# Kernel tuning notes

Measured on AMD Instinct MI355X. Metric: run time of the kernel, lower is better.

Reference implementation:

```python
import jax, jax.numpy as jnp
import numpy as np

N_HEAD = 16
D_HEAD = 64  # d_model=1024 // n_head=16


def setup_inputs() -> dict:
    key = jax.random.key(0)
    ks = jax.random.split(key, 8)
    B, S, D = 2, 2048, 1024
    scale = 1.0 / np.sqrt(D)
    return {
        "q": jax.random.normal(ks[0], (B, S, D), jnp.float32),
        "k": jax.random.normal(ks[1], (B, S, D), jnp.float32),
        "v": jax.random.normal(ks[2], (B, S, D), jnp.float32),
        "w_q": jax.random.normal(ks[3], (D, D), jnp.float32) * scale,
        "w_k": jax.random.normal(ks[4], (D, D), jnp.float32) * scale,
        "w_v": jax.random.normal(ks[5], (D, D), jnp.float32) * scale,
        "w_fc": jax.random.normal(ks[6], (D, D), jnp.float32) * scale,
        "b_fc": jnp.zeros((D,), jnp.float32),
    }


def reference(q, k, v, w_q, w_k, w_v, w_fc, b_fc):
    B, Sq, D = q.shape
    # projections (torch Linear: x @ W.T), split into heads -> [B, H, S, Dh]
    def proj(x, w):
        return (x @ w.T).reshape(B, x.shape[1], N_HEAD, D_HEAD).transpose(0, 2, 1, 3)
    qh, kh, vh = proj(q, w_q), proj(k, w_k), proj(v, w_v)
    # scaled dot-product attention with explicit weights (dropout = identity, eval mode)
    scores = jnp.einsum("bhqd,bhkd->bhqk", qh, kh) / jnp.sqrt(jnp.float32(D_HEAD))
    attn = jax.nn.softmax(scores, axis=-1)  # [B, H, Sq, Sk]
    ctx = jnp.einsum("bhqk,bhkd->bhqd", attn, vh)
    ctx = ctx.transpose(0, 2, 1, 3).reshape(B, Sq, D)
    out = ctx @ w_fc.T + b_fc
    return out, attn
```

## Files before the change

### kernel.cpp

```cpp
#include <hip/hip_runtime.h>


using f16   = _Float16;
using f16x4 = __attribute__((ext_vector_type(4))) f16;
using f16x8 = __attribute__((ext_vector_type(8))) f16;
using f32x4 = __attribute__((ext_vector_type(4))) float;

#define MFMA16(a, b, c) __builtin_amdgcn_mfma_f32_16x16x32_f16((a), (b), (c), 0, 0, 0)

__device__ static inline float fexp2(float x) {
#if __has_builtin(__builtin_amdgcn_exp2f)
  return __builtin_amdgcn_exp2f(x);
#else
  return exp2f(x);
#endif
}

#define C1 0.18033688011112042f

#define WAIT_BARRIER(IMM)                                              \
  do {                                                                 \
    asm volatile("s_waitcnt vmcnt(" #IMM ") lgkmcnt(0)" ::: "memory"); \
    __builtin_amdgcn_s_barrier();                                      \
  } while (0)

__device__ static inline void gld16(const void* gptr, void* lptr) {
  __builtin_amdgcn_global_load_lds(
      (const __attribute__((address_space(1))) void*)gptr,
      (__attribute__((address_space(3))) void*)lptr, 16, 0, 0);
}

__device__ static inline unsigned int pack2(float a, float b) {
  union { f16 h[2]; unsigned int u; } x;
  x.h[0] = (f16)a; x.h[1] = (f16)b;
  return x.u;
}

__global__ __launch_bounds__(256) void cast_all(
    const float* __restrict__ q, const float* __restrict__ k,
    const float* __restrict__ v, const float* __restrict__ wq,
    const float* __restrict__ wk, const float* __restrict__ wv,
    const float* __restrict__ wfc, f16* __restrict__ ws) {
  int i = blockIdx.x * 256 + threadIdx.x;
  const float* src;
  f16* dst;
  int li;
  if (i < 3145728) {
    if (i < 1048576)      { src = q; dst = ws;            li = i; }
    else if (i < 2097152) { src = k; dst = ws + 4194304;  li = i - 1048576; }
    else                  { src = v; dst = ws + 8388608;  li = i - 2097152; }
  } else {
    int j = i - 3145728;
    int wsel = j >> 18;
    src = (wsel == 0) ? wq : (wsel == 1) ? wk : (wsel == 2) ? wv : wfc;
    dst = ws + 12582912 + wsel * 1048576;
    li = j & 262143;
  }
  float4 x = ((const float4*)src)[li];
  f16x4 y;
  y[0] = (f16)x.x; y[1] = (f16)x.y; y[2] = (f16)x.z; y[3] = (f16)x.w;
  ((f16x4*)dst)[li] = y;
}

template <int MODE, int BN>
__global__ __launch_bounds__(256) void gemm_bt(
    const f16* __restrict__ A0, const f16* __restrict__ W0,
    const float* __restrict__ bias, void* __restrict__ Cout) {
  constexpr int FJ = BN / 32;
  __shared__ unsigned short XA[8192];
  __shared__ unsigned short WB[BN * 64];
  int tid = threadIdx.x;
  int w = tid >> 6, l = tid & 63, lq = l & 15, g = l >> 4;
  int nb3 = blockIdx.x * BN, mb = blockIdx.y * 128;
  int wsel = (MODE == 4) ? (nb3 >> 10) : 0;
  int nb = (MODE == 4) ? (nb3 & 1023) : nb3;
  const f16* A = (MODE == 4) ? A0 + (size_t)wsel * 4194304 : A0;
  const f16* W = (MODE == 4) ? W0 + (size_t)wsel * 1048576 : W0;
  bool swapR = (MODE == 4) && (wsel == 2);
  int wi = w >> 1, wj = w & 1;

  f32x4 acc[4][FJ];
#pragma unroll
  for (int i = 0; i < 4; i++)
#pragma unroll
    for (int j = 0; j < FJ; j++) acc[i][j] = (f32x4){0.f, 0.f, 0.f, 0.f};

  char* Xb = (char*)XA;
  char* Wb = (char*)WB;
  int row = tid >> 3;
  int c = (tid & 7) ^ (row & 7);
  const f16* Asrc = A + (size_t)(mb + row) * 1024 + c * 8;
  const f16* Wsrc = W + (size_t)(nb + row) * 1024 + c * 8;

  for (int k0 = 0; k0 < 1024; k0 += 64) {
#pragma unroll
    for (int i2 = 0; i2 < 4; i2++)
      gld16(Asrc + k0 + i2 * 32 * 1024, Xb + i2 * 4096 + w * 1024);
#pragma unroll
    for (int i2 = 0; i2 < BN / 32; i2++)
      gld16(Wsrc + k0 + i2 * 32 * 1024, Wb + i2 * 4096 + w * 1024);
    __syncthreads();

    const char* at = swapR ? Wb : Xb;
    const char* bt = swapR ? Xb : Wb;

    f16x8 bfr[FJ][2];
#pragma unroll
    for (int f = 0; f < FJ; f++) {
      int r = wj * (BN / 2) + f * 16 + lq;
      int sw = (r & 7) << 4;
      bfr[f][0] = *(const f16x8*)(bt + r * 128 + ((g * 16) ^ sw));
      bfr[f][1] = *(const f16x8*)(bt + r * 128 + ((64 + g * 16) ^ sw));
    }
#pragma unroll
    for (int fi = 0; fi < 4; fi++) {
      int r = wi * 64 + fi * 16 + lq;
      int sw = (r & 7) << 4;
      f16x8 a0 = *(const f16x8*)(at + r * 128 + ((g * 16) ^ sw));
      f16x8 a1 = *(const f16x8*)(at + r * 128 + ((64 + g * 16) ^ sw));
#pragma unroll
      for (int fj = 0; fj < FJ; fj++) {
        acc[fi][fj] = MFMA16(a0, bfr[fj][0], acc[fi][fj]);
        acc[fi][fj] = MFMA16(a1, bfr[fj][1], acc[fi][fj]);
      }
    }
    __syncthreads();
  }

#pragma unroll
  for (int fi = 0; fi < 4; fi++) {
#pragma unroll
    for (int fj = 0; fj < FJ; fj++) {
#pragma unroll
      for (int jj = 0; jj < 4; jj++) {
        float v = acc[fi][fj][jj];
        int iG = (swapR ? nb : mb) + wi * 64 + fi * 16 + g * 4 + jj;
        int jG = (swapR ? mb : nb) + wj * (BN / 2) + fj * 16 + lq;
        if constexpr (MODE == 3) {
          int m2 = iG, n2 = jG;
          ((float*)Cout)[(size_t)m2 * 1024 + n2] = v + bias[n2];
        } else {
          f16* dstb = (f16*)Cout + (size_t)wsel * 4194304;
          if (!swapR) {
            int m2 = iG, n2 = jG;
            size_t dst = (size_t)((m2 >> 11) * 16 + (n2 >> 6)) * 131072 +
                         (size_t)(m2 & 2047) * 64 + (n2 & 63);
            dstb[dst] = (f16)v;
          } else {
            int n2 = iG, m2 = jG;
            size_t dst = (size_t)((m2 >> 11) * 1024 + n2) * 2048 + (m2 & 2047);
            dstb[dst] = (f16)v;
          }
        }
      }
    }
  }
}

__global__ __launch_bounds__(256) void attn_fused(
    const f16* __restrict__ qh, const f16* __restrict__ kh,
    const f16* __restrict__ vt, float* __restrict__ attn,
    f16* __restrict__ ctx) {
  __shared__ unsigned short Kl0[4096], Kl1[4096];
  __shared__ unsigned short Vl0[4096], Vl1[4096];
  __shared__ unsigned short Pl[4096];
  int tid = threadIdx.x;
  int w = tid >> 6, l = tid & 63, lq = l & 15, g = l >> 4;
  int qt = blockIdx.x, bh = blockIdx.y;

  int qglob = qt * 64 + w * 16 + lq;
  const f16* qrow = qh + (size_t)(bh * 2048 + qglob) * 64;
  f16x8 qf0 = *(const f16x8*)(qrow + g * 8);
  f16x8 qf1 = *(const f16x8*)(qrow + 32 + g * 8);

  char* Kb0 = (char*)Kl0;
  char* Kb1 = (char*)Kl1;
  char* Vb0 = (char*)Vl0;
  char* Vb1 = (char*)Vl1;
  char* Pw  = (char*)Pl + w * 2048;

  int row = tid >> 3;
  int c = (tid & 7) ^ (row & 7);
  const f16* ksrc = kh + (size_t)bh * 2048 * 64 + (size_t)row * 64 + c * 8;
  const f16* vsrc = vt + (size_t)bh * 64 * 2048 + (size_t)row * 2048 + c * 8;

  int swq = (lq & 7) << 4;

  float ls = 0.f;
  gld16(ksrc,           Kb0 + w * 1024);
  gld16(ksrc + 32 * 64, Kb0 + 4096 + w * 1024);
  WAIT_BARRIER(0);
  for (int t = 0; t < 32; t++) {
    char* KbC = (t & 1) ? Kb1 : Kb0;
    char* KbN = (t & 1) ? Kb0 : Kb1;
    if (t < 31) {
      const f16* kp = ksrc + (size_t)(t + 1) * 4096;
      gld16(kp,           KbN + w * 1024);
      gld16(kp + 32 * 64, KbN + 4096 + w * 1024);
    }
#pragma unroll
    for (int cf = 0; cf < 4; cf++) {
      int kr = cf * 16 + lq;
      int sw = (kr & 7) << 4;
      f16x8 ka  = *(const f16x8*)(KbC + kr * 128 + ((g * 16) ^ sw));
      f16x8 kb2 = *(const f16x8*)(KbC + kr * 128 + ((64 + g * 16) ^ sw));
      f32x4 s = (f32x4){0.f, 0.f, 0.f, 0.f};
      s = MFMA16(ka, qf0, s);
      s = MFMA16(kb2, qf1, s);
      ls += fexp2(s[0] * C1) + fexp2(s[1] * C1) +
            fexp2(s[2] * C1) + fexp2(s[3] * C1);
    }
    WAIT_BARRIER(0);
  }
  ls += __shfl_xor(ls, 16);
  ls += __shfl_xor(ls, 32);
  float linv = 1.0f / ls;

  f32x4 acc[4];
#pragma unroll
  for (int i = 0; i < 4; i++) acc[i] = (f32x4){0.f, 0.f, 0.f, 0.f};

  float* attnrow = attn + ((size_t)bh * 2048 + qt * 64 + w * 16 + lq) * 2048;

  gld16(ksrc,             Kb0 + w * 1024);
  gld16(ksrc + 32 * 64,   Kb0 + 4096 + w * 1024);
  gld16(vsrc,             Vb0 + w * 1024);
  gld16(vsrc + 32 * 2048, Vb0 + 4096 + w * 1024);
  WAIT_BARRIER(0);
  for (int t = 0; t < 32; t++) {
    int kt = t * 64;
    char* KbC = (t & 1) ? Kb1 : Kb0;
    char* KbN = (t & 1) ? Kb0 : Kb1;
    char* VbC = (t & 1) ? Vb1 : Vb0;
    char* VbN = (t & 1) ? Vb0 : Vb1;
    if (t < 31) {
      const f16* kp = ksrc + (size_t)(t + 1) * 4096;
      const f16* vp = vsrc + (size_t)(t + 1) * 64;
      gld16(kp,             KbN + w * 1024);
      gld16(kp + 32 * 64,   KbN + 4096 + w * 1024);
      gld16(vp,             VbN + w * 1024);
      gld16(vp + 32 * 2048, VbN + 4096 + w * 1024);
    }

#pragma unroll
    for (int cf = 0; cf < 4; cf++) {
      int kr = cf * 16 + lq;
      int sw = (kr & 7) << 4;
      f16x8 ka  = *(const f16x8*)(KbC + kr * 128 + ((g * 16) ^ sw));
      f16x8 kb2 = *(const f16x8*)(KbC + kr * 128 + ((64 + g * 16) ^ sw));
      f32x4 s = (f32x4){0.f, 0.f, 0.f, 0.f};
      s = MFMA16(ka, qf0, s);
      s = MFMA16(kb2, qf1, s);
      float e0 = fexp2(s[0] * C1) * linv;
      float e1 = fexp2(s[1] * C1) * linv;
      float e2 = fexp2(s[2] * C1) * linv;
      float e3 = fexp2(s[3] * C1) * linv;
      float4 o = {e0, e1, e2, e3};
      *(float4*)(attnrow + kt + cf * 16 + g * 4) = o;
      int k0 = cf * 16 + g * 4;
      *(unsigned int*)(Pw + lq * 128 + ((k0 * 2) ^ swq))       = pack2(e0, e1);
      *(unsigned int*)(Pw + lq * 128 + (((k0 + 2) * 2) ^ swq)) = pack2(e2, e3);
    }

    {
      f16x8 pb0 = *(const f16x8*)(Pw + lq * 128 + ((g * 16) ^ swq));
      f16x8 pb1 = *(const f16x8*)(Pw + lq * 128 + ((64 + g * 16) ^ swq));
#pragma unroll
      for (int af = 0; af < 4; af++) {
        int vr = af * 16 + lq;
        int sv = (vr & 7) << 4;
        f16x8 va0 = *(const f16x8*)(VbC + vr * 128 + ((g * 16) ^ sv));
        f16x8 va1 = *(const f16x8*)(VbC + vr * 128 + ((64 + g * 16) ^ sv));
        acc[af] = MFMA16(va0, pb0, acc[af]);
        acc[af] = MFMA16(va1, pb1, acc[af]);
      }
    }
    WAIT_BARRIER(4);
  }

#pragma unroll
  for (int af = 0; af < 4; af++) {
#pragma unroll
    for (int jj = 0; jj < 4; jj += 2) {
      int dh0 = af * 16 + g * 4 + jj;
      *(unsigned int*)(Pw + lq * 128 + ((dh0 * 2) ^ swq)) =
          pack2(acc[af][jj], acc[af][jj + 1]);
    }
  }
  {
    int q2 = l >> 2, cc = l & 3;
    int swr = (q2 & 7) << 4;
    int b = bh >> 4, h = bh & 15;
    f16* crow = ctx + ((size_t)b * 2048 + qt * 64 + w * 16 + q2) * 1024 + h * 64;
#pragma unroll
    for (int t2 = 0; t2 < 2; t2++) {
      f16x8 v2 = *(const f16x8*)(Pw + q2 * 128 + ((cc * 32 + t2 * 16) ^ swr));
      *(f16x8*)(crow + cc * 16 + t2 * 8) = v2;
    }
  }
}

extern "C" void kernel_launch(void* const* d_in, const int* in_sizes, int n_in,
                              void* d_out, int out_size, void* d_ws,
                              size_t ws_size, hipStream_t stream) {
  (void)in_sizes; (void)n_in; (void)out_size; (void)ws_size;
  const float* q   = (const float*)d_in[0];
  const float* k   = (const float*)d_in[1];
  const float* v   = (const float*)d_in[2];
  const float* wq  = (const float*)d_in[3];
  const float* wk  = (const float*)d_in[4];
  const float* wv  = (const float*)d_in[5];
  const float* wfc = (const float*)d_in[6];
  const float* bfc = (const float*)d_in[7];

  f16* ws = (f16*)d_ws;
  f16* qf   = ws;
  f16* wqf  = ws + 12582912;
  f16* wfcf = ws + 15728640;
  f16* qhp  = ws + 16777216;
  f16* khp  = ws + 20971520;
  f16* vtp  = ws + 25165824;
  f16* ctxp = ws + 29360128;

  float* outp  = (float*)d_out;
  float* attnp = outp + 4194304;

  cast_all<<<16384, 256, 0, stream>>>(q, k, v, wq, wk, wv, wfc, ws);
  gemm_bt<4, 128><<<dim3(24, 32), 256, 0, stream>>>(qf, wqf, nullptr, qhp);
  attn_fused<<<dim3(32, 32), 256, 0, stream>>>(qhp, khp, vtp, attnp, ctxp);
  gemm_bt<3, 64><<<dim3(16, 32), 256, 0, stream>>>(ctxp, wfcf, bfc, outp);
}
```

Before: 288.1 us.

## Process 32 query rows per wave and remap blocks to XCDs in attention

Each wave of the fused attention kernel now handles two 16-row query fragments, so a block covers 128 queries instead of 64. Every K/V tile loaded into LDS is reused across twice as many queries, which halves the grid and the K/V traffic. The 1-D grid is also remapped so that consecutive block IDs on the same XCD share a batch-head, aiming for better L2 locality. In exchange, register pressure rises with doubled accumulators, the P buffer doubles in LDS, and there are fewer blocks (512) to fill the GPU.

```diff
diff --git a/kernel.cpp b/kernel.cpp
--- a/kernel.cpp
+++ b/kernel.cpp
@@ -157,27 +157,34 @@
   }
 }
 
-__global__ __launch_bounds__(256) void attn_fused(
+__global__ __launch_bounds__(256, 2) void attn_fused(
     const f16* __restrict__ qh, const f16* __restrict__ kh,
     const f16* __restrict__ vt, float* __restrict__ attn,
     f16* __restrict__ ctx) {
   __shared__ unsigned short Kl0[4096], Kl1[4096];
   __shared__ unsigned short Vl0[4096], Vl1[4096];
-  __shared__ unsigned short Pl[4096];
+  __shared__ unsigned short Pl[8192];
   int tid = threadIdx.x;
   int w = tid >> 6, l = tid & 63, lq = l & 15, g = l >> 4;
-  int qt = blockIdx.x, bh = blockIdx.y;
-
-  int qglob = qt * 64 + w * 16 + lq;
-  const f16* qrow = qh + (size_t)(bh * 2048 + qglob) * 64;
-  f16x8 qf0 = *(const f16x8*)(qrow + g * 8);
-  f16x8 qf1 = *(const f16x8*)(qrow + 32 + g * 8);
+
+  int bid = blockIdx.x;
+  int xcd = bid & 7, j = bid >> 3;
+  int bh = xcd * 4 + (j >> 4);
+  int qt = j & 15;
+
+  const f16* qbase = qh + (size_t)(bh * 2048 + qt * 128 + w * 32 + lq) * 64;
+  f16x8 qf[2][2];
+#pragma unroll
+  for (int f = 0; f < 2; f++) {
+    qf[f][0] = *(const f16x8*)(qbase + f * 16 * 64 + g * 8);
+    qf[f][1] = *(const f16x8*)(qbase + f * 16 * 64 + 32 + g * 8);
+  }
 
   char* Kb0 = (char*)Kl0;
   char* Kb1 = (char*)Kl1;
   char* Vb0 = (char*)Vl0;
   char* Vb1 = (char*)Vl1;
-  char* Pw  = (char*)Pl + w * 2048;
+  char* Pw  = (char*)Pl + w * 4096;
 
   int row = tid >> 3;
   int c = (tid & 7) ^ (row & 7);
@@ -186,7 +193,7 @@
 
   int swq = (lq & 7) << 4;
 
-  float ls = 0.f;
+  float ls[2] = {0.f, 0.f};
   gld16(ksrc,           Kb0 + w * 1024);
   gld16(ksrc + 32 * 64, Kb0 + 4096 + w * 1024);
   WAIT_BARRIER(0);
@@ -204,23 +211,35 @@
       int sw = (kr & 7) << 4;
       f16x8 ka  = *(const f16x8*)(KbC + kr * 128 + ((g * 16) ^ sw));
       f16x8 kb2 = *(const f16x8*)(KbC + kr * 128 + ((64 + g * 16) ^ sw));
-      f32x4 s = (f32x4){0.f, 0.f, 0.f, 0.f};
-      s = MFMA16(ka, qf0, s);
-      s = MFMA16(kb2, qf1, s);
-      ls += fexp2(s[0] * C1) + fexp2(s[1] * C1) +
-            fexp2(s[2] * C1) + fexp2(s[3] * C1);
+#pragma unroll
+      for (int f = 0; f < 2; f++) {
+        f32x4 s = (f32x4){0.f, 0.f, 0.f, 0.f};
+        s = MFMA16(ka, qf[f][0], s);
+        s = MFMA16(kb2, qf[f][1], s);
+        ls[f] += fexp2(s[0] * C1) + fexp2(s[1] * C1) +
+                 fexp2(s[2] * C1) + fexp2(s[3] * C1);
+      }
     }
     WAIT_BARRIER(0);
   }
-  ls += __shfl_xor(ls, 16);
-  ls += __shfl_xor(ls, 32);
-  float linv = 1.0f / ls;
-
-  f32x4 acc[4];
-#pragma unroll
-  for (int i = 0; i < 4; i++) acc[i] = (f32x4){0.f, 0.f, 0.f, 0.f};
-
-  float* attnrow = attn + ((size_t)bh * 2048 + qt * 64 + w * 16 + lq) * 2048;
+  float linv[2];
+#pragma unroll
+  for (int f = 0; f < 2; f++) {
+    float t = ls[f];
+    t += __shfl_xor(t, 16);
+    t += __shfl_xor(t, 32);
+    linv[f] = 1.0f / t;
+  }
+
+  f32x4 acc[2][4];
+#pragma unroll
+  for (int f = 0; f < 2; f++)
+#pragma unroll
+    for (int i = 0; i < 4; i++) acc[f][i] = (f32x4){0.f, 0.f, 0.f, 0.f};
+
+  float* attnrow0 =
+      attn + ((size_t)bh * 2048 + qt * 128 + w * 32 + lq) * 2048;
+  float* attnrow1 = attnrow0 + 16 * 2048;
 
   gld16(ksrc,             Kb0 + w * 1024);
   gld16(ksrc + 32 * 64,   Kb0 + 4096 + w * 1024);
@@ -248,54 +267,71 @@
       int sw = (kr & 7) << 4;
       f16x8 ka  = *(const f16x8*)(KbC + kr * 128 + ((g * 16) ^ sw));
       f16x8 kb2 = *(const f16x8*)(KbC + kr * 128 + ((64 + g * 16) ^ sw));
-      f32x4 s = (f32x4){0.f, 0.f, 0.f, 0.f};
-      s = MFMA16(ka, qf0, s);
-      s = MFMA16(kb2, qf1, s);
-      float e0 = fexp2(s[0] * C1) * linv;
-      float e1 = fexp2(s[1] * C1) * linv;
-      float e2 = fexp2(s[2] * C1) * linv;
-      float e3 = fexp2(s[3] * C1) * linv;
-      float4 o = {e0, e1, e2, e3};
-      *(float4*)(attnrow + kt + cf * 16 + g * 4) = o;
       int k0 = cf * 16 + g * 4;
-      *(unsigned int*)(Pw + lq * 128 + ((k0 * 2) ^ swq))       = pack2(e0, e1);
-      *(unsigned int*)(Pw + lq * 128 + (((k0 + 2) * 2) ^ swq)) = pack2(e2, e3);
+#pragma unroll
+      for (int f = 0; f < 2; f++) {
+        f32x4 s = (f32x4){0.f, 0.f, 0.f, 0.f};
+        s = MFMA16(ka, qf[f][0], s);
+        s = MFMA16(kb2, qf[f][1], s);
+        float e0 = fexp2(s[0] * C1) * linv[f];
+        float e1 = fexp2(s[1] * C1) * linv[f];
+        float e2 = fexp2(s[2] * C1) * linv[f];
+        float e3 = fexp2(s[3] * C1) * linv[f];
+        float4 o = {e0, e1, e2, e3};
+        *(float4*)((f ? attnrow1 : attnrow0) + kt + cf * 16 + g * 4) = o;
+        char* Pr = Pw + (f * 16 + lq) * 128;
+        *(unsigned int*)(Pr + ((k0 * 2) ^ swq))       = pack2(e0, e1);
+        *(unsigned int*)(Pr + (((k0 + 2) * 2) ^ swq)) = pack2(e2, e3);
+      }
     }
 
     {
-      f16x8 pb0 = *(const f16x8*)(Pw + lq * 128 + ((g * 16) ^ swq));
-      f16x8 pb1 = *(const f16x8*)(Pw + lq * 128 + ((64 + g * 16) ^ swq));
+      f16x8 pb[2][2];
+#pragma unroll
+      for (int f = 0; f < 2; f++) {
+        char* Pr = Pw + (f * 16 + lq) * 128;
+        pb[f][0] = *(const f16x8*)(Pr + ((g * 16) ^ swq));
+        pb[f][1] = *(const f16x8*)(Pr + ((64 + g * 16) ^ swq));
+      }
 #pragma unroll
       for (int af = 0; af < 4; af++) {
         int vr = af * 16 + lq;
         int sv = (vr & 7) << 4;
         f16x8 va0 = *(const f16x8*)(VbC + vr * 128 + ((g * 16) ^ sv));
         f16x8 va1 = *(const f16x8*)(VbC + vr * 128 + ((64 + g * 16) ^ sv));
-        acc[af] = MFMA16(va0, pb0, acc[af]);
-        acc[af] = MFMA16(va1, pb1, acc[af]);
-      }
-    }
-    WAIT_BARRIER(4);
-  }
-
-#pragma unroll
-  for (int af = 0; af < 4; af++) {
-#pragma unroll
-    for (int jj = 0; jj < 4; jj += 2) {
-      int dh0 = af * 16 + g * 4 + jj;
-      *(unsigned int*)(Pw + lq * 128 + ((dh0 * 2) ^ swq)) =
-          pack2(acc[af][jj], acc[af][jj + 1]);
+#pragma unroll
+        for (int f = 0; f < 2; f++) {
+          acc[f][af] = MFMA16(va0, pb[f][0], acc[f][af]);
+          acc[f][af] = MFMA16(va1, pb[f][1], acc[f][af]);
+        }
+      }
+    }
+    WAIT_BARRIER(8);
+  }
+
+#pragma unroll
+  for (int f = 0; f < 2; f++) {
+    char* Pr = Pw + (f * 16 + lq) * 128;
+#pragma unroll
+    for (int af = 0; af < 4; af++) {
+#pragma unroll
+      for (int jj = 0; jj < 4; jj += 2) {
+        int dh0 = af * 16 + g * 4 + jj;
+        *(unsigned int*)(Pr + ((dh0 * 2) ^ swq)) =
+            pack2(acc[f][af][jj], acc[f][af][jj + 1]);
+      }
     }
   }
   {
-    int q2 = l >> 2, cc = l & 3;
+    int q2 = l >> 1, cc = l & 1;
     int swr = (q2 & 7) << 4;
     int b = bh >> 4, h = bh & 15;
-    f16* crow = ctx + ((size_t)b * 2048 + qt * 64 + w * 16 + q2) * 1024 + h * 64;
-#pragma unroll
-    for (int t2 = 0; t2 < 2; t2++) {
-      f16x8 v2 = *(const f16x8*)(Pw + q2 * 128 + ((cc * 32 + t2 * 16) ^ swr));
-      *(f16x8*)(crow + cc * 16 + t2 * 8) = v2;
+    f16* crow =
+        ctx + ((size_t)b * 2048 + qt * 128 + w * 32 + q2) * 1024 + h * 64;
+#pragma unroll
+    for (int t2 = 0; t2 < 4; t2++) {
+      f16x8 v2 = *(const f16x8*)(Pw + q2 * 128 + ((cc * 64 + t2 * 16) ^ swr));
+      *(f16x8*)(crow + cc * 32 + t2 * 8) = v2;
     }
   }
 }
@@ -327,6 +363,6 @@
 
   cast_all<<<16384, 256, 0, stream>>>(q, k, v, wq, wk, wv, wfc, ws);
   gemm_bt<4, 128><<<dim3(24, 32), 256, 0, stream>>>(qf, wqf, nullptr, qhp);
-  attn_fused<<<dim3(32, 32), 256, 0, stream>>>(qhp, khp, vtp, attnp, ctxp);
+  attn_fused<<<512, 256, 0, stream>>>(qhp, khp, vtp, attnp, ctxp);
   gemm_bt<3, 64><<<dim3(16, 32), 256, 0, stream>>>(ctxp, wfcf, bfc, outp);
 }
```

Measured after the change: 282.0 us. -2.1%, faster.

## Compute attention in a single pass with split-K across waves and deferred normalization

Applied to the files above, without the earlier changes.

Replaces the two-pass attention (one pass for row sums, one recomputing scores to write normalized probabilities) with a single pass. Each block takes 16 query rows, and its 8 waves each cover a 256-key slice. Unnormalized exp values are kept in LDS, wave partial sums are reduced in shared memory, and P·V partials are combined through LDS atomics. The attn matrix is then written normalized with nontemporal stores. This removes the duplicate QK^T and exp work and the K/V LDS staging, at the cost of reading K/V straight from global memory, using more LDS per block, and doing shared atomics.

```diff
diff --git a/kernel.cpp b/kernel.cpp
--- a/kernel.cpp
+++ b/kernel.cpp
@@ -17,12 +17,6 @@
 }
 
 #define C1 0.18033688011112042f
-
-#define WAIT_BARRIER(IMM)                                              \
-  do {                                                                 \
-    asm volatile("s_waitcnt vmcnt(" #IMM ") lgkmcnt(0)" ::: "memory"); \
-    __builtin_amdgcn_s_barrier();                                      \
-  } while (0)
 
 __device__ static inline void gld16(const void* gptr, void* lptr) {
   __builtin_amdgcn_global_load_lds(
@@ -157,146 +151,124 @@
   }
 }
 
-__global__ __launch_bounds__(256) void attn_fused(
+__global__ __launch_bounds__(512, 4) void attn_one(
     const f16* __restrict__ qh, const f16* __restrict__ kh,
     const f16* __restrict__ vt, float* __restrict__ attn,
     f16* __restrict__ ctx) {
-  __shared__ unsigned short Kl0[4096], Kl1[4096];
-  __shared__ unsigned short Vl0[4096], Vl1[4096];
-  __shared__ unsigned short Pl[4096];
+  __shared__ unsigned short Pl[8][4096];
+  __shared__ float CT[16][64];
+  __shared__ float LV[8][16];
+  __shared__ float LI[16];
   int tid = threadIdx.x;
   int w = tid >> 6, l = tid & 63, lq = l & 15, g = l >> 4;
-  int qt = blockIdx.x, bh = blockIdx.y;
-
-  int qglob = qt * 64 + w * 16 + lq;
-  const f16* qrow = qh + (size_t)(bh * 2048 + qglob) * 64;
+
+  int bid = blockIdx.x;
+  int xcd = bid & 7, j = bid >> 3;
+  int bh = xcd * 4 + (j >> 7);
+  int rt = j & 127;
+  int rowbase = rt * 16;
+
+  if (tid < 256) {
+    float* ctf = (float*)CT;
+    ctf[tid] = 0.f; ctf[tid + 256] = 0.f; ctf[tid + 512] = 0.f;
+    ctf[tid + 768] = 0.f;
+  }
+
+  const f16* qrow = qh + ((size_t)bh * 2048 + rowbase + lq) * 64;
   f16x8 qf0 = *(const f16x8*)(qrow + g * 8);
   f16x8 qf1 = *(const f16x8*)(qrow + 32 + g * 8);
 
-  char* Kb0 = (char*)Kl0;
-  char* Kb1 = (char*)Kl1;
-  char* Vb0 = (char*)Vl0;
-  char* Vb1 = (char*)Vl1;
-  char* Pw  = (char*)Pl + w * 2048;
-
-  int row = tid >> 3;
-  int c = (tid & 7) ^ (row & 7);
-  const f16* ksrc = kh + (size_t)bh * 2048 * 64 + (size_t)row * 64 + c * 8;
-  const f16* vsrc = vt + (size_t)bh * 64 * 2048 + (size_t)row * 2048 + c * 8;
-
-  int swq = (lq & 7) << 4;
+  const f16* kbh = kh + (size_t)bh * 131072;
+  const f16* vbh = vt + (size_t)bh * 131072;
+  char* Pw = (char*)Pl[w];
+  int swz = (lq & 7) << 4;
+  int kc0 = w * 256;
 
   float ls = 0.f;
-  gld16(ksrc,           Kb0 + w * 1024);
-  gld16(ksrc + 32 * 64, Kb0 + 4096 + w * 1024);
-  WAIT_BARRIER(0);
-  for (int t = 0; t < 32; t++) {
-    char* KbC = (t & 1) ? Kb1 : Kb0;
-    char* KbN = (t & 1) ? Kb0 : Kb1;
-    if (t < 31) {
-      const f16* kp = ksrc + (size_t)(t + 1) * 4096;
-      gld16(kp,           KbN + w * 1024);
-      gld16(kp + 32 * 64, KbN + 4096 + w * 1024);
-    }
+  f32x4 acc[4];
+#pragma unroll
+  for (int i = 0; i < 4; i++) acc[i] = (f32x4){0.f, 0.f, 0.f, 0.f};
+
+  for (int t = 0; t < 4; t++) {
+    int kt = kc0 + t * 64;
+    int tl2 = t * 128;
 #pragma unroll
     for (int cf = 0; cf < 4; cf++) {
-      int kr = cf * 16 + lq;
-      int sw = (kr & 7) << 4;
-      f16x8 ka  = *(const f16x8*)(KbC + kr * 128 + ((g * 16) ^ sw));
-      f16x8 kb2 = *(const f16x8*)(KbC + kr * 128 + ((64 + g * 16) ^ sw));
+      const f16* kr = kbh + (size_t)(kt + cf * 16 + lq) * 64 + g * 8;
+      f16x8 ka  = *(const f16x8*)kr;
+      f16x8 kb2 = *(const f16x8*)(kr + 32);
       f32x4 s = (f32x4){0.f, 0.f, 0.f, 0.f};
       s = MFMA16(ka, qf0, s);
       s = MFMA16(kb2, qf1, s);
-      ls += fexp2(s[0] * C1) + fexp2(s[1] * C1) +
-            fexp2(s[2] * C1) + fexp2(s[3] * C1);
-    }
-    WAIT_BARRIER(0);
-  }
+      float e0 = fexp2(s[0] * C1);
+      float e1 = fexp2(s[1] * C1);
+      float e2 = fexp2(s[2] * C1);
+      float e3 = fexp2(s[3] * C1);
+      ls += (e0 + e1) + (e2 + e3);
+      int k0b = tl2 + (cf * 16 + g * 4) * 2;
+      *(unsigned int*)(Pw + lq * 512 + (k0b ^ swz))       = pack2(e0, e1);
+      *(unsigned int*)(Pw + lq * 512 + ((k0b + 4) ^ swz)) = pack2(e2, e3);
+    }
+    f16x8 pb0 = *(const f16x8*)(Pw + lq * 512 + ((tl2 + g * 16) ^ swz));
+    f16x8 pb1 = *(const f16x8*)(Pw + lq * 512 + ((tl2 + 64 + g * 16) ^ swz));
+#pragma unroll
+    for (int af = 0; af < 4; af++) {
+      const f16* vr = vbh + (size_t)(af * 16 + lq) * 2048 + kt + g * 8;
+      f16x8 va0 = *(const f16x8*)vr;
+      f16x8 va1 = *(const f16x8*)(vr + 32);
+      acc[af] = MFMA16(va0, pb0, acc[af]);
+      acc[af] = MFMA16(va1, pb1, acc[af]);
+    }
+  }
+
   ls += __shfl_xor(ls, 16);
   ls += __shfl_xor(ls, 32);
-  float linv = 1.0f / ls;
-
-  f32x4 acc[4];
-#pragma unroll
-  for (int i = 0; i < 4; i++) acc[i] = (f32x4){0.f, 0.f, 0.f, 0.f};
-
-  float* attnrow = attn + ((size_t)bh * 2048 + qt * 64 + w * 16 + lq) * 2048;
-
-  gld16(ksrc,             Kb0 + w * 1024);
-  gld16(ksrc + 32 * 64,   Kb0 + 4096 + w * 1024);
-  gld16(vsrc,             Vb0 + w * 1024);
-  gld16(vsrc + 32 * 2048, Vb0 + 4096 + w * 1024);
-  WAIT_BARRIER(0);
-  for (int t = 0; t < 32; t++) {
-    int kt = t * 64;
-    char* KbC = (t & 1) ? Kb1 : Kb0;
-    char* KbN = (t & 1) ? Kb0 : Kb1;
-    char* VbC = (t & 1) ? Vb1 : Vb0;
-    char* VbN = (t & 1) ? Vb0 : Vb1;
-    if (t < 31) {
-      const f16* kp = ksrc + (size_t)(t + 1) * 4096;
-      const f16* vp = vsrc + (size_t)(t + 1) * 64;
-      gld16(kp,             KbN + w * 1024);
-      gld16(kp + 32 * 64,   KbN + 4096 + w * 1024);
-      gld16(vp,             VbN + w * 1024);
-      gld16(vp + 32 * 2048, VbN + 4096 + w * 1024);
-    }
-
-#pragma unroll
-    for (int cf = 0; cf < 4; cf++) {
-      int kr = cf * 16 + lq;
-      int sw = (kr & 7) << 4;
-      f16x8 ka  = *(const f16x8*)(KbC + kr * 128 + ((g * 16) ^ sw));
-      f16x8 kb2 = *(const f16x8*)(KbC + kr * 128 + ((64 + g * 16) ^ sw));
-      f32x4 s = (f32x4){0.f, 0.f, 0.f, 0.f};
-      s = MFMA16(ka, qf0, s);
-      s = MFMA16(kb2, qf1, s);
-      float e0 = fexp2(s[0] * C1) * linv;
-      float e1 = fexp2(s[1] * C1) * linv;
-      float e2 = fexp2(s[2] * C1) * linv;
-      float e3 = fexp2(s[3] * C1) * linv;
-      float4 o = {e0, e1, e2, e3};
-      *(float4*)(attnrow + kt + cf * 16 + g * 4) = o;
-      int k0 = cf * 16 + g * 4;
-      *(unsigned int*)(Pw + lq * 128 + ((k0 * 2) ^ swq))       = pack2(e0, e1);
-      *(unsigned int*)(Pw + lq * 128 + (((k0 + 2) * 2) ^ swq)) = pack2(e2, e3);
-    }
-
-    {
-      f16x8 pb0 = *(const f16x8*)(Pw + lq * 128 + ((g * 16) ^ swq));
-      f16x8 pb1 = *(const f16x8*)(Pw + lq * 128 + ((64 + g * 16) ^ swq));
-#pragma unroll
-      for (int af = 0; af < 4; af++) {
-        int vr = af * 16 + lq;
-        int sv = (vr & 7) << 4;
-        f16x8 va0 = *(const f16x8*)(VbC + vr * 128 + ((g * 16) ^ sv));
-        f16x8 va1 = *(const f16x8*)(VbC + vr * 128 + ((64 + g * 16) ^ sv));
-        acc[af] = MFMA16(va0, pb0, acc[af]);
-        acc[af] = MFMA16(va1, pb1, acc[af]);
-      }
-    }
-    WAIT_BARRIER(4);
-  }
-
-#pragma unroll
-  for (int af = 0; af < 4; af++) {
-#pragma unroll
-    for (int jj = 0; jj < 4; jj += 2) {
-      int dh0 = af * 16 + g * 4 + jj;
-      *(unsigned int*)(Pw + lq * 128 + ((dh0 * 2) ^ swq)) =
-          pack2(acc[af][jj], acc[af][jj + 1]);
-    }
-  }
+  if (l < 16) LV[w][l] = ls;
+  __syncthreads();
+  if (tid < 16) {
+    float s2 = 0.f;
+#pragma unroll
+    for (int w2 = 0; w2 < 8; w2++) s2 += LV[w2][tid];
+    LI[tid] = 1.0f / s2;
+  }
+  __syncthreads();
+
   {
-    int q2 = l >> 2, cc = l & 3;
-    int swr = (q2 & 7) << 4;
+    float sc = LI[lq];
+#pragma unroll
+    for (int af = 0; af < 4; af++)
+#pragma unroll
+      for (int jj = 0; jj < 4; jj++)
+        atomicAdd(&CT[lq][af * 16 + g * 4 + jj], acc[af][jj] * sc);
+  }
+
+  {
+    int r = tid >> 5, sl = tid & 31;
+    float li = LI[r];
+    int rs = (r & 7) << 4;
+    const char* Pbase = (const char*)Pl + r * 512;
+    float* arow = attn + ((size_t)bh * 2048 + rowbase + r) * 2048;
+#pragma unroll
+    for (int i = 0; i < 16; i++) {
+      int col = i * 128 + sl * 4;
+      int w2 = col >> 8;
+      int lb = (col & 255) * 2;
+      f16x4 pv = *(const f16x4*)(Pbase + w2 * 8192 + (lb ^ rs));
+      f32x4 o = {(float)pv[0] * li, (float)pv[1] * li,
+                 (float)pv[2] * li, (float)pv[3] * li};
+      __builtin_nontemporal_store(o, (f32x4*)(arow + col));
+    }
+  }
+  __syncthreads();
+
+  if (tid < 256) {
+    int q2 = tid >> 4, d0 = (tid & 15) * 4;
+    float4 c = *(const float4*)&CT[q2][d0];
     int b = bh >> 4, h = bh & 15;
-    f16* crow = ctx + ((size_t)b * 2048 + qt * 64 + w * 16 + q2) * 1024 + h * 64;
-#pragma unroll
-    for (int t2 = 0; t2 < 2; t2++) {
-      f16x8 v2 = *(const f16x8*)(Pw + q2 * 128 + ((cc * 32 + t2 * 16) ^ swr));
-      *(f16x8*)(crow + cc * 16 + t2 * 8) = v2;
-    }
+    f16* crow = ctx + ((size_t)b * 2048 + rowbase + q2) * 1024 + h * 64 + d0;
+    f16x4 y;
+    y[0] = (f16)c.x; y[1] = (f16)c.y; y[2] = (f16)c.z; y[3] = (f16)c.w;
+    *(f16x4*)crow = y;
   }
 }
 
@@ -327,6 +299,6 @@
 
   cast_all<<<16384, 256, 0, stream>>>(q, k, v, wq, wk, wv, wfc, ws);
   gemm_bt<4, 128><<<dim3(24, 32), 256, 0, stream>>>(qf, wqf, nullptr, qhp);
-  attn_fused<<<dim3(32, 32), 256, 0, stream>>>(qhp, khp, vtp, attnp, ctxp);
+  attn_one<<<4096, 512, 0, stream>>>(qhp, khp, vtp, attnp, ctxp);
   gemm_bt<3, 64><<<dim3(16, 32), 256, 0, stream>>>(ctxp, wfcf, bfc, outp);
 }
```

After: 477.7 us. 1.66x slower.
